# Kernel optimization log

Measured on AMD Instinct MI355X. Metric: run time of the kernel, lower is better.

Reference implementation:

```python
import jax, jax.numpy as jnp
import numpy as np

B, C, H, W = 4, 64, 96, 96
HEAD_SIZE = 4


def setup_inputs() -> dict:
    key = jax.random.key(0)
    ks = jax.random.split(key, 9)
    s = 1.0 / np.sqrt(C)
    d = {"x": jax.random.normal(ks[0], (B, C, H, W), dtype=jnp.float32)}
    for i, name in enumerate(["Wq", "Wk", "Wv", "Wo"]):
        d[name] = jax.random.normal(ks[1 + i], (C, C), dtype=jnp.float32) * s
    for i, name in enumerate(["bq", "bk", "bv", "bo"]):
        d[name] = jax.random.normal(ks[5 + i], (C,), dtype=jnp.float32) * 0.01
    return d


def reference(x, Wq, bq, Wk, bk, Wv, bv, Wo, bo):
    b, c, h, w = x.shape
    hw = h * w
    hs = HEAD_SIZE
    S = hw // hs  # spatial tokens per head (heads split along HW, not channels)
    scale = 1.0 / jnp.sqrt(jnp.asarray(hs, x.dtype))

    def proj(y, Wm, bias):  # 1x1 conv == per-pixel channel matmul
        return jnp.einsum('bchw,oc->bohw', y, Wm) + bias[None, :, None, None]

    def heads(y):  # (B,C,H,W) -> (B,hs,C,S)
        return y.reshape(b, c, hs, S).transpose(0, 2, 1, 3)

    q = heads(proj(x, Wq, bq))  # (B,hs,C,S)
    k = heads(proj(x, Wk, bk))  # (B,hs,C,S)
    v = heads(proj(x, Wv, bv))  # (B,hs,C,S)

    # attention = softmax(q^T k / sqrt(head_size)) over last axis: (B,hs,S,S)
    attn = jax.nn.softmax(jnp.einsum('bhcs,bhct->bhst', q, k) * scale, axis=-1)
    # out = v @ attn^T : (B,hs,C,S)
    out = jnp.einsum('bhcs,bhts->bhct', v, attn)
    # torch .reshape on the (B,hs,C,S) layout -> (B,C,H,W); jnp.reshape matches
    out = out.reshape(b, c, h, w)
    out = jnp.einsum('bchw,oc->bohw', out, Wo) + bo[None, :, None, None]
    return x + out
```

## Files before the change

kernel.cpp:

```cpp
#include <hip/hip_runtime.h>
#include <stdint.h>

#define HW_  9216
#define S_   2304
#define NBH  16
#define NSPLIT 3
#define JPS  12
#define NPART ((size_t)NBH * S_ * 64)
#define SCALE_LOG2E 0.72134752044448169136f

using f32x4 = __attribute__((ext_vector_type(4))) float;
using u32x4 = __attribute__((ext_vector_type(4))) uint32_t;
using u32x2 = __attribute__((ext_vector_type(2))) uint32_t;
using s16x8 = __attribute__((ext_vector_type(8))) short;

typedef const __attribute__((address_space(1))) void gbl_void;
typedef __attribute__((address_space(3))) void lds_void;

__device__ __forceinline__ uint32_t pkbf(float lo, float hi) {
    uint32_t r;
    asm("v_cvt_pk_bf16_f32 %0, %1, %2" : "=v"(r) : "v"(lo), "v"(hi));
    return r;
}
__device__ __forceinline__ float bf2f(uint16_t h) {
    return __builtin_bit_cast(float, (uint32_t)h << 16);
}

__global__ __launch_bounds__(64) void qkv_proj(
    const float* __restrict__ x,
    const float* __restrict__ Wq, const float* __restrict__ Wk, const float* __restrict__ Wv,
    const float* __restrict__ bq, const float* __restrict__ bk, const float* __restrict__ bv,
    uint16_t* __restrict__ Qo, uint16_t* __restrict__ Ko, uint16_t* __restrict__ Vo)
{
    const int mode = blockIdx.y;
    const float* W    = (mode == 0) ? Wq : (mode == 1) ? Wk : Wv;
    const float* bias = (mode == 0) ? bq : (mode == 1) ? bk : bv;
    const float ws = (mode == 0) ? SCALE_LOG2E : 1.0f;

    const int pix0 = blockIdx.x * 64;
    const int b   = pix0 / HW_;
    const int hw0 = pix0 % HW_;
    const int h   = hw0 / S_;
    const int s0  = hw0 % S_;
    const int bh  = b * 4 + h;

    const int lane = threadIdx.x;
    const int g = lane >> 4, lr = lane & 15;

    __shared__ alignas(16) uint16_t xt[64 * 64];

    {
        const float* xb = x + (size_t)b * 64 * HW_ + hw0 + lane;
        uint32_t rp[32];
        #pragma unroll
        for (int cc = 0; cc < 32; ++cc)
            rp[cc] = pkbf(xb[(size_t)(2 * cc) * HW_], xb[(size_t)(2 * cc + 1) * HW_]);
        #pragma unroll
        for (int cb = 0; cb < 8; ++cb) {
            u32x4 d = { rp[cb * 4], rp[cb * 4 + 1], rp[cb * 4 + 2], rp[cb * 4 + 3] };
            *(u32x4*)(xt + lane * 64 + 8 * (cb ^ (lane & 7))) = d;
        }
    }
    __syncthreads();

    s16x8 wf[4][2];
    #pragma unroll
    for (int t4 = 0; t4 < 4; ++t4)
        #pragma unroll
        for (int ks = 0; ks < 2; ++ks) {
            const float* wp = W + (t4 * 16 + lr) * 64 + ks * 32 + g * 8;
            f32x4 w0 = *(const f32x4*)wp;
            f32x4 w1 = *(const f32x4*)(wp + 4);
            u32x4 d = { pkbf(w0[0] * ws, w0[1] * ws), pkbf(w0[2] * ws, w0[3] * ws),
                        pkbf(w1[0] * ws, w1[1] * ws), pkbf(w1[2] * ws, w1[3] * ws) };
            wf[t4][ks] = __builtin_bit_cast(s16x8, d);
        }

    s16x8 xf[4][2];
    #pragma unroll
    for (int pt = 0; pt < 4; ++pt)
        #pragma unroll
        for (int ks = 0; ks < 2; ++ks) {
            const int pix = pt * 16 + lr;
            xf[pt][ks] = *(const s16x8*)(xt + pix * 64 + 8 * ((ks * 4 + g) ^ (pix & 7)));
        }

    f32x4 acc[4][4];
    if (mode != 2) {
        #pragma unroll
        for (int mt = 0; mt < 4; ++mt) {
            f32x4 bi = *(const f32x4*)(bias + mt * 16 + g * 4);
            bi *= ws;
            #pragma unroll
            for (int nt = 0; nt < 4; ++nt) acc[mt][nt] = bi;
        }
        #pragma unroll
        for (int ks = 0; ks < 2; ++ks)
            #pragma unroll
            for (int mt = 0; mt < 4; ++mt)
                #pragma unroll
                for (int nt = 0; nt < 4; ++nt)
                    acc[mt][nt] = __builtin_amdgcn_mfma_f32_16x16x32_bf16(
                        wf[mt][ks], xf[nt][ks], acc[mt][nt], 0, 0, 0);
        uint16_t* dst = ((mode == 0) ? Qo : Ko) + ((size_t)bh * S_ + s0) * 64;
        #pragma unroll
        for (int mt = 0; mt < 4; ++mt)
            #pragma unroll
            for (int nt = 0; nt < 4; ++nt) {
                uint32_t d0 = pkbf(acc[mt][nt][0], acc[mt][nt][1]);
                uint32_t d1 = pkbf(acc[mt][nt][2], acc[mt][nt][3]);
                const int o = mt * 16 + g * 4;
                *(uint32_t*)(dst + (nt * 16 + lr) * 64 + o)     = d0;
                *(uint32_t*)(dst + (nt * 16 + lr) * 64 + o + 2) = d1;
            }
    } else {
        #pragma unroll
        for (int nt = 0; nt < 4; ++nt) {
            const float bv = bias[nt * 16 + lr];
            #pragma unroll
            for (int mt = 0; mt < 4; ++mt) acc[mt][nt] = (f32x4){bv, bv, bv, bv};
        }
        #pragma unroll
        for (int ks = 0; ks < 2; ++ks)
            #pragma unroll
            for (int mt = 0; mt < 4; ++mt)
                #pragma unroll
                for (int nt = 0; nt < 4; ++nt)
                    acc[mt][nt] = __builtin_amdgcn_mfma_f32_16x16x32_bf16(
                        xf[mt][ks], wf[nt][ks], acc[mt][nt], 0, 0, 0);
        uint16_t* dst = Vo + (size_t)bh * 64 * S_;
        #pragma unroll
        for (int mt = 0; mt < 4; ++mt)
            #pragma unroll
            for (int nt = 0; nt < 4; ++nt) {
                uint32_t d0 = pkbf(acc[mt][nt][0], acc[mt][nt][1]);
                uint32_t d1 = pkbf(acc[mt][nt][2], acc[mt][nt][3]);
                const int o = nt * 16 + lr;
                const int sb = s0 + mt * 16 + g * 4;
                *(uint32_t*)(dst + (size_t)o * S_ + sb)     = d0;
                *(uint32_t*)(dst + (size_t)o * S_ + sb + 2) = d1;
            }
    }
}

__global__ __launch_bounds__(256, 3) void attn(
    const uint16_t* __restrict__ Qg, const uint16_t* __restrict__ Kg,
    const uint16_t* __restrict__ Vg, uint16_t* __restrict__ Op,
    float* __restrict__ Lp)
{
    const int blk = blockIdx.x;
    const int xcd = blk & 7;
    const int i   = blk >> 3;
    const int bh  = xcd * 2 + (i & 1);
    const int i2  = i >> 1;
    const int sp  = i2 % 3;
    const int qb  = i2 / 3;
    const int j0  = sp * JPS;
    const int b   = bh >> 2;
    const int h   = bh & 3;

    const int tid  = threadIdx.x;
    const int wave = tid >> 6;
    const int lane = tid & 63;
    const int g    = lane >> 4;
    const int lr   = lane & 15;
    const int q0   = qb * 128 + wave * 32;

    __shared__ alignas(16) uint16_t Kl[4096];
    __shared__ alignas(16) uint16_t Vl[4096];
    __shared__ alignas(16) uint16_t Pw[4][2304];
    uint16_t* P = Pw[wave];

    const uint16_t* Qb = Qg + (size_t)bh * S_ * 64;
    const uint16_t* Kb = Kg + (size_t)bh * S_ * 64;
    const uint16_t* Vb = Vg + (size_t)bh * 64 * S_;

    s16x8 qf[2][2];
    #pragma unroll
    for (int qt = 0; qt < 2; ++qt)
        #pragma unroll
        for (int ks = 0; ks < 2; ++ks)
            qf[qt][ks] = *(const s16x8*)(Qb + (size_t)(q0 + qt * 16 + lr) * 64 + ks * 32 + g * 8);

    f32x4 oacc[2][4];
    float l_r[2][4];
    #pragma unroll
    for (int qt = 0; qt < 2; ++qt) {
        #pragma unroll
        for (int ct = 0; ct < 4; ++ct) oacc[qt][ct] = (f32x4){0.f, 0.f, 0.f, 0.f};
        #pragma unroll
        for (int r = 0; r < 4; ++r) l_r[qt][r] = 0.f;
    }

    for (int jj = 0; jj < JPS; ++jj) {
        const int j = j0 + jj;
        #pragma unroll
        for (int call = 0; call < 2; ++call) {
            const int chunk = wave * 128 + call * 64 + lane;
            const int row   = chunk >> 3;
            const int cb    = (chunk & 7) ^ (row & 7);
            __builtin_amdgcn_global_load_lds(
                (gbl_void*)(Kb + ((size_t)(j * 64 + row) * 64 + cb * 8)),
                (lds_void*)(Kl + (wave * 128 + call * 64) * 8), 16, 0, 0);
            __builtin_amdgcn_global_load_lds(
                (gbl_void*)(Vb + ((size_t)row * S_ + j * 64 + cb * 8)),
                (lds_void*)(Vl + (wave * 128 + call * 64) * 8), 16, 0, 0);
        }
        asm volatile("s_waitcnt vmcnt(0)" ::: "memory");
        __syncthreads();

        f32x4 sacc[2][4];
        #pragma unroll
        for (int qt = 0; qt < 2; ++qt)
            #pragma unroll
            for (int kt = 0; kt < 4; ++kt) sacc[qt][kt] = (f32x4){0.f, 0.f, 0.f, 0.f};
        #pragma unroll
        for (int ks = 0; ks < 2; ++ks)
            #pragma unroll
            for (int kt = 0; kt < 4; ++kt) {
                const int key = kt * 16 + lr;
                s16x8 kf = *(const s16x8*)(&Kl[key * 64 + 8 * ((ks * 4 + g) ^ (key & 7))]);
                sacc[0][kt] = __builtin_amdgcn_mfma_f32_16x16x32_bf16(qf[0][ks], kf, sacc[0][kt], 0, 0, 0);
                sacc[1][kt] = __builtin_amdgcn_mfma_f32_16x16x32_bf16(qf[1][ks], kf, sacc[1][kt], 0, 0, 0);
            }

        #pragma unroll
        for (int qt = 0; qt < 2; ++qt)
            #pragma unroll
            for (int kt = 0; kt < 4; ++kt)
                #pragma unroll
                for (int r = 0; r < 4; ++r) {
                    const float pv = __builtin_amdgcn_exp2f(sacc[qt][kt][r]);
                    l_r[qt][r] += pv;
                    P[(qt * 16 + 4 * g + r) * 72 + kt * 16 + lr] = (uint16_t)pkbf(pv, pv);
                }

        #pragma unroll
        for (int ks = 0; ks < 2; ++ks) {
            s16x8 pf0 = *(const s16x8*)(P + (0 * 16 + lr) * 72 + ks * 32 + g * 8);
            s16x8 pf1 = *(const s16x8*)(P + (1 * 16 + lr) * 72 + ks * 32 + g * 8);
            #pragma unroll
            for (int ct = 0; ct < 4; ++ct) {
                const int c = ct * 16 + lr;
                s16x8 vf = *(const s16x8*)(&Vl[c * 64 + 8 * ((ks * 4 + g) ^ (c & 7))]);
                oacc[0][ct] = __builtin_amdgcn_mfma_f32_16x16x32_bf16(pf0, vf, oacc[0][ct], 0, 0, 0);
                oacc[1][ct] = __builtin_amdgcn_mfma_f32_16x16x32_bf16(pf1, vf, oacc[1][ct], 0, 0, 0);
            }
        }

        __syncthreads();
    }

    #pragma unroll
    for (int mask = 1; mask < 16; mask <<= 1) {
        #pragma unroll
        for (int qt = 0; qt < 2; ++qt)
            #pragma unroll
            for (int r = 0; r < 4; ++r)
                l_r[qt][r] += __shfl_xor(l_r[qt][r], mask, 64);
    }

    #pragma unroll
    for (int qt = 0; qt < 2; ++qt)
        #pragma unroll
        for (int ct = 0; ct < 4; ++ct) {
            uint32_t d0 = pkbf(oacc[qt][ct][0], oacc[qt][ct][1]);
            uint32_t d1 = pkbf(oacc[qt][ct][2], oacc[qt][ct][3]);
            const int base = (ct * 16 + lr) * 36 + qt * 16 + 4 * g;
            *(uint32_t*)(P + base)     = d0;
            *(uint32_t*)(P + base + 2) = d1;
        }
    __syncthreads();

    const int c = lane;
    u32x2 wv[8];
    #pragma unroll
    for (int e = 0; e < 8; ++e)
        wv[e] = *(const u32x2*)(P + c * 36 + e * 4);
    uint16_t* dst = Op + (size_t)sp * NPART
                  + ((size_t)(b * 64 + h * 16 + (c >> 2)) * HW_ + (c & 3) * S_ + q0);
    #pragma unroll
    for (int s4 = 0; s4 < 4; ++s4) {
        u32x4 d = { wv[2 * s4][0], wv[2 * s4][1], wv[2 * s4 + 1][0], wv[2 * s4 + 1][1] };
        *(u32x4*)(dst + s4 * 8) = d;
    }

    if (lr == 0) {
        #pragma unroll
        for (int qt = 0; qt < 2; ++qt)
            #pragma unroll
            for (int r = 0; r < 4; ++r)
                Lp[((size_t)sp * NBH + bh) * S_ + q0 + qt * 16 + 4 * g + r] = l_r[qt][r];
    }
}

__global__ __launch_bounds__(64) void out_proj(
    const uint16_t* __restrict__ Op, const float* __restrict__ Lp,
    const float* __restrict__ x,
    const float* __restrict__ Wo, const float* __restrict__ bo,
    float* __restrict__ out)
{
    const int pix0 = blockIdx.x * 64;
    const int b   = pix0 / HW_;
    const int hw0 = pix0 % HW_;
    const int lane = threadIdx.x;
    const int g = lane >> 4, lr = lane & 15;
    const int t = (hw0 % S_) + lane;

    __shared__ alignas(16) uint16_t at[64 * 64];

    float inv[4];
    #pragma unroll
    for (int hh = 0; hh < 4; ++hh) {
        float sl = 0.f;
        #pragma unroll
        for (int sp2 = 0; sp2 < NSPLIT; ++sp2)
            sl += Lp[((size_t)sp2 * NBH + b * 4 + hh) * S_ + t];
        inv[hh] = 1.0f / sl;
    }

    {
        const size_t base = (size_t)b * 64 * HW_ + hw0 + lane;
        uint32_t rp[32];
        #pragma unroll
        for (int cc = 0; cc < 32; ++cc) {
            float a0 = 0.f, a1 = 0.f;
            #pragma unroll
            for (int sp2 = 0; sp2 < NSPLIT; ++sp2) {
                const size_t o2 = (size_t)sp2 * NPART + base;
                a0 += bf2f(Op[o2 + (size_t)(2 * cc) * HW_]);
                a1 += bf2f(Op[o2 + (size_t)(2 * cc + 1) * HW_]);
            }
            rp[cc] = pkbf(a0 * inv[(2 * cc) >> 4], a1 * inv[(2 * cc + 1) >> 4]);
        }
        #pragma unroll
        for (int cb = 0; cb < 8; ++cb) {
            u32x4 d = { rp[cb * 4], rp[cb * 4 + 1], rp[cb * 4 + 2], rp[cb * 4 + 3] };
            *(u32x4*)(at + lane * 64 + 8 * (cb ^ (lane & 7))) = d;
        }
    }
    __syncthreads();

    s16x8 wf[4][2];
    #pragma unroll
    for (int t4 = 0; t4 < 4; ++t4)
        #pragma unroll
        for (int ks = 0; ks < 2; ++ks) {
            const float* wp = Wo + (t4 * 16 + lr) * 64 + ks * 32 + g * 8;
            f32x4 w0 = *(const f32x4*)wp;
            f32x4 w1 = *(const f32x4*)(wp + 4);
            u32x4 d = { pkbf(w0[0], w0[1]), pkbf(w0[2], w0[3]),
                        pkbf(w1[0], w1[1]), pkbf(w1[2], w1[3]) };
            wf[t4][ks] = __builtin_bit_cast(s16x8, d);
        }

    s16x8 af[4][2];
    #pragma unroll
    for (int pt = 0; pt < 4; ++pt)
        #pragma unroll
        for (int ks = 0; ks < 2; ++ks) {
            const int pix = pt * 16 + lr;
            af[pt][ks] = *(const s16x8*)(at + pix * 64 + 8 * ((ks * 4 + g) ^ (pix & 7)));
        }

    f32x4 acc[4][4];
    #pragma unroll
    for (int mt = 0; mt < 4; ++mt) {
        f32x4 bi = *(const f32x4*)(bo + mt * 16 + g * 4);
        #pragma unroll
        for (int nt = 0; nt < 4; ++nt) acc[mt][nt] = bi;
    }
    #pragma unroll
    for (int ks = 0; ks < 2; ++ks)
        #pragma unroll
        for (int mt = 0; mt < 4; ++mt)
            #pragma unroll
            for (int nt = 0; nt < 4; ++nt)
                acc[mt][nt] = __builtin_amdgcn_mfma_f32_16x16x32_bf16(
                    wf[mt][ks], af[nt][ks], acc[mt][nt], 0, 0, 0);

    #pragma unroll
    for (int mt = 0; mt < 4; ++mt)
        #pragma unroll
        for (int nt = 0; nt < 4; ++nt) {
            const int o = mt * 16 + g * 4;
            const size_t rowb = ((size_t)(b * 64 + o)) * HW_ + hw0 + nt * 16 + lr;
            #pragma unroll
            for (int r = 0; r < 4; ++r) {
                const size_t a2 = rowb + (size_t)r * HW_;
                out[a2] = acc[mt][nt][r] + x[a2];
            }
        }
}

extern "C" void kernel_launch(void* const* d_in, const int* in_sizes, int n_in,
                              void* d_out, int out_size, void* d_ws, size_t ws_size,
                              hipStream_t stream) {
    const float* x  = (const float*)d_in[0];
    const float* Wq = (const float*)d_in[1];
    const float* Wk = (const float*)d_in[2];
    const float* Wv = (const float*)d_in[3];
    const float* Wo = (const float*)d_in[4];
    const float* bq = (const float*)d_in[5];
    const float* bk = (const float*)d_in[6];
    const float* bv = (const float*)d_in[7];
    const float* bo = (const float*)d_in[8];
    float* out = (float*)d_out;

    uint16_t* Q  = (uint16_t*)d_ws;
    uint16_t* K  = Q + NPART;
    uint16_t* V  = K + NPART;
    uint16_t* Op = V + NPART;
    float*    Lp = (float*)(Op + (size_t)NSPLIT * NPART);

    qkv_proj<<<dim3(576, 3), 64, 0, stream>>>(x, Wq, Wk, Wv, bq, bk, bv, Q, K, V);
    attn<<<864, 256, 0, stream>>>(Q, K, V, Op, Lp);
    out_proj<<<576, 64, 0, stream>>>(Op, Lp, x, Wo, bo, out);
}
```

Baseline: 68.85 us.

## Raise attention KV split to four and split projections across output-channel halves

Attention now splits the key range four ways instead of three (1152 blocks instead of 864), raising parallelism and shortening each block's serial loop. The QKV and output projection kernels each gain a grid dimension that splits the 64 output channels into two halves, doubling block count while each block computes half the MFMA tiles. The cost is that each projection block still loads and transposes the full 64-channel input tile, so that global read work doubles. The extra partial-output split also means more partial O and L traffic to write and then reduce in out_proj.

```diff
diff --git a/kernel.cpp b/kernel.cpp
--- a/kernel.cpp
+++ b/kernel.cpp
@@ -4,8 +4,8 @@
 #define HW_  9216
 #define S_   2304
 #define NBH  16
-#define NSPLIT 3
-#define JPS  12
+#define NSPLIT 4
+#define JPS  9
 #define NPART ((size_t)NBH * S_ * 64)
 #define SCALE_LOG2E 0.72134752044448169136f
 
@@ -33,6 +33,7 @@
     uint16_t* __restrict__ Qo, uint16_t* __restrict__ Ko, uint16_t* __restrict__ Vo)
 {
     const int mode = blockIdx.y;
+    const int o0   = blockIdx.z * 32;
     const float* W    = (mode == 0) ? Wq : (mode == 1) ? Wk : Wv;
     const float* bias = (mode == 0) ? bq : (mode == 1) ? bk : bv;
     const float ws = (mode == 0) ? SCALE_LOG2E : 1.0f;
@@ -63,17 +64,17 @@
     }
     __syncthreads();
 
-    s16x8 wf[4][2];
-    #pragma unroll
-    for (int t4 = 0; t4 < 4; ++t4)
+    s16x8 wf[2][2];
+    #pragma unroll
+    for (int t2 = 0; t2 < 2; ++t2)
         #pragma unroll
         for (int ks = 0; ks < 2; ++ks) {
-            const float* wp = W + (t4 * 16 + lr) * 64 + ks * 32 + g * 8;
+            const float* wp = W + (o0 + t2 * 16 + lr) * 64 + ks * 32 + g * 8;
             f32x4 w0 = *(const f32x4*)wp;
             f32x4 w1 = *(const f32x4*)(wp + 4);
             u32x4 d = { pkbf(w0[0] * ws, w0[1] * ws), pkbf(w0[2] * ws, w0[3] * ws),
                         pkbf(w1[0] * ws, w1[1] * ws), pkbf(w1[2] * ws, w1[3] * ws) };
-            wf[t4][ks] = __builtin_bit_cast(s16x8, d);
+            wf[t2][ks] = __builtin_bit_cast(s16x8, d);
         }
 
     s16x8 xf[4][2];
@@ -85,11 +86,11 @@
             xf[pt][ks] = *(const s16x8*)(xt + pix * 64 + 8 * ((ks * 4 + g) ^ (pix & 7)));
         }
 
-    f32x4 acc[4][4];
     if (mode != 2) {
-        #pragma unroll
-        for (int mt = 0; mt < 4; ++mt) {
-            f32x4 bi = *(const f32x4*)(bias + mt * 16 + g * 4);
+        f32x4 acc[2][4];
+        #pragma unroll
+        for (int mt = 0; mt < 2; ++mt) {
+            f32x4 bi = *(const f32x4*)(bias + o0 + mt * 16 + g * 4);
             bi *= ws;
             #pragma unroll
             for (int nt = 0; nt < 4; ++nt) acc[mt][nt] = bi;
@@ -97,26 +98,27 @@
         #pragma unroll
         for (int ks = 0; ks < 2; ++ks)
             #pragma unroll
-            for (int mt = 0; mt < 4; ++mt)
+            for (int mt = 0; mt < 2; ++mt)
                 #pragma unroll
                 for (int nt = 0; nt < 4; ++nt)
                     acc[mt][nt] = __builtin_amdgcn_mfma_f32_16x16x32_bf16(
                         wf[mt][ks], xf[nt][ks], acc[mt][nt], 0, 0, 0);
         uint16_t* dst = ((mode == 0) ? Qo : Ko) + ((size_t)bh * S_ + s0) * 64;
         #pragma unroll
-        for (int mt = 0; mt < 4; ++mt)
+        for (int mt = 0; mt < 2; ++mt)
             #pragma unroll
             for (int nt = 0; nt < 4; ++nt) {
                 uint32_t d0 = pkbf(acc[mt][nt][0], acc[mt][nt][1]);
                 uint32_t d1 = pkbf(acc[mt][nt][2], acc[mt][nt][3]);
-                const int o = mt * 16 + g * 4;
+                const int o = o0 + mt * 16 + g * 4;
                 *(uint32_t*)(dst + (nt * 16 + lr) * 64 + o)     = d0;
                 *(uint32_t*)(dst + (nt * 16 + lr) * 64 + o + 2) = d1;
             }
     } else {
-        #pragma unroll
-        for (int nt = 0; nt < 4; ++nt) {
-            const float bv = bias[nt * 16 + lr];
+        f32x4 acc[4][2];
+        #pragma unroll
+        for (int nt = 0; nt < 2; ++nt) {
+            const float bv = bias[o0 + nt * 16 + lr];
             #pragma unroll
             for (int mt = 0; mt < 4; ++mt) acc[mt][nt] = (f32x4){bv, bv, bv, bv};
         }
@@ -125,17 +127,17 @@
             #pragma unroll
             for (int mt = 0; mt < 4; ++mt)
                 #pragma unroll
-                for (int nt = 0; nt < 4; ++nt)
+                for (int nt = 0; nt < 2; ++nt)
                     acc[mt][nt] = __builtin_amdgcn_mfma_f32_16x16x32_bf16(
                         xf[mt][ks], wf[nt][ks], acc[mt][nt], 0, 0, 0);
         uint16_t* dst = Vo + (size_t)bh * 64 * S_;
         #pragma unroll
         for (int mt = 0; mt < 4; ++mt)
             #pragma unroll
-            for (int nt = 0; nt < 4; ++nt) {
+            for (int nt = 0; nt < 2; ++nt) {
                 uint32_t d0 = pkbf(acc[mt][nt][0], acc[mt][nt][1]);
                 uint32_t d1 = pkbf(acc[mt][nt][2], acc[mt][nt][3]);
-                const int o = nt * 16 + lr;
+                const int o = o0 + nt * 16 + lr;
                 const int sb = s0 + mt * 16 + g * 4;
                 *(uint32_t*)(dst + (size_t)o * S_ + sb)     = d0;
                 *(uint32_t*)(dst + (size_t)o * S_ + sb + 2) = d1;
@@ -153,8 +155,8 @@
     const int i   = blk >> 3;
     const int bh  = xcd * 2 + (i & 1);
     const int i2  = i >> 1;
-    const int sp  = i2 % 3;
-    const int qb  = i2 / 3;
+    const int sp  = i2 & 3;
+    const int qb  = i2 >> 2;
     const int j0  = sp * JPS;
     const int b   = bh >> 2;
     const int h   = bh & 3;
@@ -301,6 +303,7 @@
     float* __restrict__ out)
 {
     const int pix0 = blockIdx.x * 64;
+    const int o0   = blockIdx.y * 32;
     const int b   = pix0 / HW_;
     const int hw0 = pix0 % HW_;
     const int lane = threadIdx.x;
@@ -341,17 +344,17 @@
     }
     __syncthreads();
 
-    s16x8 wf[4][2];
-    #pragma unroll
-    for (int t4 = 0; t4 < 4; ++t4)
+    s16x8 wf[2][2];
+    #pragma unroll
+    for (int t2 = 0; t2 < 2; ++t2)
         #pragma unroll
         for (int ks = 0; ks < 2; ++ks) {
-            const float* wp = Wo + (t4 * 16 + lr) * 64 + ks * 32 + g * 8;
+            const float* wp = Wo + (o0 + t2 * 16 + lr) * 64 + ks * 32 + g * 8;
             f32x4 w0 = *(const f32x4*)wp;
             f32x4 w1 = *(const f32x4*)(wp + 4);
             u32x4 d = { pkbf(w0[0], w0[1]), pkbf(w0[2], w0[3]),
                         pkbf(w1[0], w1[1]), pkbf(w1[2], w1[3]) };
-            wf[t4][ks] = __builtin_bit_cast(s16x8, d);
+            wf[t2][ks] = __builtin_bit_cast(s16x8, d);
         }
 
     s16x8 af[4][2];
@@ -363,27 +366,27 @@
             af[pt][ks] = *(const s16x8*)(at + pix * 64 + 8 * ((ks * 4 + g) ^ (pix & 7)));
         }
 
-    f32x4 acc[4][4];
-    #pragma unroll
-    for (int mt = 0; mt < 4; ++mt) {
-        f32x4 bi = *(const f32x4*)(bo + mt * 16 + g * 4);
+    f32x4 acc[2][4];
+    #pragma unroll
+    for (int mt = 0; mt < 2; ++mt) {
+        f32x4 bi = *(const f32x4*)(bo + o0 + mt * 16 + g * 4);
         #pragma unroll
         for (int nt = 0; nt < 4; ++nt) acc[mt][nt] = bi;
     }
     #pragma unroll
     for (int ks = 0; ks < 2; ++ks)
         #pragma unroll
-        for (int mt = 0; mt < 4; ++mt)
+        for (int mt = 0; mt < 2; ++mt)
             #pragma unroll
             for (int nt = 0; nt < 4; ++nt)
                 acc[mt][nt] = __builtin_amdgcn_mfma_f32_16x16x32_bf16(
                     wf[mt][ks], af[nt][ks], acc[mt][nt], 0, 0, 0);
 
     #pragma unroll
-    for (int mt = 0; mt < 4; ++mt)
+    for (int mt = 0; mt < 2; ++mt)
         #pragma unroll
         for (int nt = 0; nt < 4; ++nt) {
-            const int o = mt * 16 + g * 4;
+            const int o = o0 + mt * 16 + g * 4;
             const size_t rowb = ((size_t)(b * 64 + o)) * HW_ + hw0 + nt * 16 + lr;
             #pragma unroll
             for (int r = 0; r < 4; ++r) {
@@ -413,7 +416,7 @@
     uint16_t* Op = V + NPART;
     float*    Lp = (float*)(Op + (size_t)NSPLIT * NPART);
 
-    qkv_proj<<<dim3(576, 3), 64, 0, stream>>>(x, Wq, Wk, Wv, bq, bk, bv, Q, K, V);
-    attn<<<864, 256, 0, stream>>>(Q, K, V, Op, Lp);
-    out_proj<<<576, 64, 0, stream>>>(Op, Lp, x, Wo, bo, out);
-}
+    qkv_proj<<<dim3(576, 3, 2), 64, 0, stream>>>(x, Wq, Wk, Wv, bq, bk, bv, Q, K, V);
+    attn<<<1152, 256, 0, stream>>>(Q, K, V, Op, Lp);
+    out_proj<<<dim3(576, 2), 64, 0, stream>>>(Op, Lp, x, Wo, bo, out);
+}
```

Result: no change. 68.40 us (-0.7%).
